# Kernel optimization log

Measured on AMD Instinct MI355X. Metric: run time of the kernel, lower is better.

## Reference

```python
import jax, jax.numpy as jnp
import numpy as np

B, S, D = 1, 4096, 1024
H = 16
DH = D // H  # 64
THETA = 10000.0


def setup_inputs() -> dict:
    key = jax.random.key(0)
    kq, kk, kv, kwq, kwk, kwv, kwo = jax.random.split(key, 7)
    scale = 0.02
    return {
        "q": jax.random.normal(kq, (B, S, D), dtype=jnp.float32),
        "k": jax.random.normal(kk, (B, S, D), dtype=jnp.float32),
        "v": jax.random.normal(kv, (B, S, D), dtype=jnp.float32),
        "Wq": jax.random.normal(kwq, (D, D), dtype=jnp.float32) * scale,
        "Wk": jax.random.normal(kwk, (D, D), dtype=jnp.float32) * scale,
        "Wv": jax.random.normal(kwv, (D, D), dtype=jnp.float32) * scale,
        "Wo": jax.random.normal(kwo, (D, D), dtype=jnp.float32) * scale,
        "bo": jnp.zeros((D,), dtype=jnp.float32),
    }


def _rope_tables(seq_len, d_head, dtype):
    # freqs_cis = polar(1, outer(t, 1/theta^(2i/d)))  -> cos/sin tables [seq, d_head//2]
    inv_freq = 1.0 / (THETA ** (jnp.arange(0, d_head, 2, dtype=jnp.float32) / d_head))
    ang = jnp.arange(seq_len, dtype=jnp.float32)[:, None] * inv_freq[None, :]
    return jnp.cos(ang).astype(dtype), jnp.sin(ang).astype(dtype)


def _apply_rope(x, cos, sin):
    # x: [B, S, H, DH]; pairs (even, odd) form complex numbers (xr + i*xi)
    xr = x[..., 0::2]
    xi = x[..., 1::2]
    c = cos[None, :, None, :]
    s = sin[None, :, None, :]
    out_r = xr * c - xi * s
    out_i = xr * s + xi * c
    # interleave back: [..., DH//2, 2] -> [..., DH]
    return jnp.stack([out_r, out_i], axis=-1).reshape(x.shape)


def reference(q, k, v, Wq, Wk, Wv, Wo, bo):
    b, sq, d = q.shape
    sk = k.shape[1]
    # torch nn.Linear: y = x @ W.T (no bias for q/k/v)
    xq = (q @ Wq.T).reshape(b, sq, H, DH)
    xk = (k @ Wk.T).reshape(b, sk, H, DH)
    xv = (v @ Wv.T).reshape(b, sk, H, DH)

    cos, sin = _rope_tables(max(sq, sk), DH, q.dtype)
    xq = _apply_rope(xq, cos[:sq], sin[:sq])
    xk = _apply_rope(xk, cos[:sk], sin[:sk])

    scale = 1.0 / np.sqrt(DH)
    # naive unfused attention (as in the source): full score matrix [B,H,Sq,Sk]
    scores = jnp.einsum("bqhd,bkhd->bhqk", xq, xk) * scale
    attn = jax.nn.softmax(scores, axis=-1)
    out = jnp.einsum("bhqk,bkhd->bqhd", attn, xv)
    out = out.reshape(b, sq, d)
    # output projection (with bias); dropout is identity in eval
    return out @ Wo.T + bo
```

## Files before the change

kernel.cpp:

```cpp
#include <hip/hip_runtime.h>
#include <hip/hip_bf16.h>
#include <math.h>

#define SQ 4096
#define DM 1024
#define NH 16

typedef unsigned int uint32;
typedef unsigned short u16;
typedef __attribute__((ext_vector_type(8))) __bf16 bf16x8;
typedef __attribute__((ext_vector_type(4))) __bf16 bf16x4;
typedef __attribute__((ext_vector_type(4))) float f32x4;
typedef __attribute__((ext_vector_type(4))) short s16x4;
typedef __attribute__((ext_vector_type(8))) unsigned short u16x8;
typedef __attribute__((ext_vector_type(4))) unsigned short u16x4;

__device__ __forceinline__ u16 f2bf(float f) {
  uint32 u = __builtin_bit_cast(uint32, f);
  u += 0x7FFFu + ((u >> 16) & 1u);
  return (u16)(u >> 16);
}

__device__ __forceinline__ void gld16(const void* g, void* l) {
  __builtin_amdgcn_global_load_lds((const __attribute__((address_space(1))) void*)g,
                                   (__attribute__((address_space(3))) void*)l, 16, 0, 0);
}

__device__ __forceinline__ f32x4 mfma32(bf16x8 a, bf16x8 b, f32x4 c) {
  return __builtin_amdgcn_mfma_f32_16x16x32_bf16(a, b, c, 0, 0, 0);
}

__device__ __forceinline__ f32x4 mfma16(s16x4 a, s16x4 b, f32x4 c) {
  return __builtin_amdgcn_mfma_f32_16x16x16bf16_1k(a, b, c, 0, 0, 0);
}

__global__ void cvt_kernel(const float* __restrict__ src, u16* __restrict__ dst, int n4, float scale) {
  int i = blockIdx.x * blockDim.x + threadIdx.x;
  if (i < n4) {
    float4 v = reinterpret_cast<const float4*>(src)[i];
    u16x4 o = { f2bf(v.x * scale), f2bf(v.y * scale), f2bf(v.z * scale), f2bf(v.w * scale) };
    reinterpret_cast<u16x4*>(dst)[i] = o;
  }
}

__global__ void rope_tab_kernel(float2* __restrict__ tab) {
  int t = blockIdx.x * blockDim.x + threadIdx.x;
  int s = t >> 5, p = t & 31;
  double inv = pow(10000.0, -(double)p / 32.0);
  float ang = (float)s * (float)inv;
  tab[t] = make_float2(cosf(ang), sinf(ang));
}

__device__ __forceinline__ void gemm_core(const u16* __restrict__ Ag, const u16* __restrict__ Bg,
                                          u16* As, u16* Bs, f32x4 (&acc)[4][4], int s0, int i0) {
  const int tid = threadIdx.x;
  const int lane = tid & 63;
  const int wv = tid >> 6;
  const int wr = wv >> 1, wc = wv & 1;
  const int r15 = lane & 15, g = lane >> 4;
  const int srow = tid >> 2;
  const int schk = (tid & 3) * 8;

  for (int k0 = 0; k0 < DM; k0 += 32) {
#pragma unroll
    for (int half = 0; half < 2; ++half) {
      gld16(Ag + (size_t)(s0 + half * 64 + srow) * DM + k0 + schk, As + (half * 256 + wv * 64) * 8);
      gld16(Bg + (size_t)(i0 + half * 64 + srow) * DM + k0 + schk, Bs + (half * 256 + wv * 64) * 8);
    }
    __syncthreads();
    bf16x8 af[4], bfr[4];
#pragma unroll
    for (int m = 0; m < 4; ++m)
      af[m] = *reinterpret_cast<const bf16x8*>(As + (wr * 64 + m * 16 + r15) * 32 + g * 8);
#pragma unroll
    for (int n = 0; n < 4; ++n)
      bfr[n] = *reinterpret_cast<const bf16x8*>(Bs + (wc * 64 + n * 16 + r15) * 32 + g * 8);
#pragma unroll
    for (int m = 0; m < 4; ++m)
#pragma unroll
      for (int n = 0; n < 4; ++n)
        acc[m][n] = mfma32(af[m], bfr[n], acc[m][n]);
    __syncthreads();
  }
}

__global__ __launch_bounds__(256) void proj_kernel(
    const u16* __restrict__ qb, const u16* __restrict__ kb, const u16* __restrict__ vb,
    const u16* __restrict__ Wq, const u16* __restrict__ Wk, const u16* __restrict__ Wv,
    u16* __restrict__ Xq, u16* __restrict__ Xk, u16* __restrict__ Vt,
    const float2* __restrict__ tab) {
  __shared__ u16 As[128 * 32], Bs[128 * 32];
  const int z = blockIdx.z;
  const u16* Ag = (z == 0) ? qb : (z == 1) ? kb : vb;
  const u16* Bg = (z == 0) ? Wq : (z == 1) ? Wk : Wv;
  const int s0 = blockIdx.x * 128, i0 = blockIdx.y * 128;
  f32x4 acc[4][4] = {};
  gemm_core(Ag, Bg, As, Bs, acc, s0, i0);

  const int tid = threadIdx.x, lane = tid & 63, wv = tid >> 6;
  const int wr = wv >> 1, wc = wv & 1, r15 = lane & 15, g = lane >> 4;
  if (z < 2) {
    u16* dst = (z == 0) ? Xq : Xk;
#pragma unroll
    for (int m = 0; m < 4; ++m) {
#pragma unroll
      for (int n = 0; n < 4; ++n) {
        int i = i0 + wc * 64 + n * 16 + r15;
        int p = (i & 63) >> 1;
#pragma unroll
        for (int r = 0; r < 4; ++r) {
          int s = s0 + wr * 64 + m * 16 + g * 4 + r;
          float v = acc[m][n][r];
          float o = __shfl_xor(v, 1);
          float2 cs = tab[s * 32 + p];
          float res = ((lane & 1) == 0) ? (v * cs.x - o * cs.y)
                                        : (o * cs.y + v * cs.x);
          dst[(size_t)s * DM + i] = f2bf(res);
        }
      }
    }
  } else {
#pragma unroll
    for (int m = 0; m < 4; ++m) {
#pragma unroll
      for (int n = 0; n < 4; ++n) {
        int i = i0 + wc * 64 + n * 16 + r15;
        int h = i >> 6, dh = i & 63;
        int sb = s0 + wr * 64 + m * 16 + g * 4;
        u16x4 pk = { f2bf(acc[m][n][0]), f2bf(acc[m][n][1]), f2bf(acc[m][n][2]), f2bf(acc[m][n][3]) };
        *reinterpret_cast<u16x4*>(Vt + (size_t)h * (64 * SQ) + (size_t)dh * SQ + sb) = pk;
      }
    }
  }
}

__global__ __launch_bounds__(256) void attn_kernel(const u16* __restrict__ Xq, const u16* __restrict__ Xk,
                                                   const u16* __restrict__ Vt, u16* __restrict__ Ob) {
  __shared__ u16 Ks[64 * 64], Vs[64 * 64];
  const int tid = threadIdx.x, lane = tid & 63, wv = tid >> 6;
  const int r15 = lane & 15, g = lane >> 4;
  const int h = blockIdx.y;
  const int q0 = blockIdx.x * 64 + wv * 16;

  bf16x8 qf[2];
#pragma unroll
  for (int kc = 0; kc < 2; ++kc)
    qf[kc] = *reinterpret_cast<const bf16x8*>(Xq + (size_t)(q0 + r15) * DM + h * 64 + kc * 32 + g * 8);

  f32x4 oacc[4] = {};
  float m_run = -3e38f, l_run = 0.f;

  u16x8 kst[2], vst[2];
  auto ldregs = [&](int t) {
#pragma unroll
    for (int j = 0; j < 2; ++j) {
      int c = tid + j * 256, row = c >> 3, ch = c & 7;
      kst[j] = *reinterpret_cast<const u16x8*>(Xk + (size_t)(t * 64 + row) * DM + h * 64 + ch * 8);
      vst[j] = *reinterpret_cast<const u16x8*>(Vt + (size_t)h * (64 * SQ) + (size_t)row * SQ + t * 64 + ch * 8);
    }
  };
  ldregs(0);

  for (int t = 0; t < 64; ++t) {
    __syncthreads();
#pragma unroll
    for (int j = 0; j < 2; ++j) {
      int c = tid + j * 256, row = c >> 3, ch = c & 7;
      int byt = (row * 128 + ch * 16) ^ ((row & 7) << 4);
      *reinterpret_cast<u16x8*>(reinterpret_cast<char*>(Ks) + byt) = kst[j];
      *reinterpret_cast<u16x8*>(reinterpret_cast<char*>(Vs) + byt) = vst[j];
    }
    __syncthreads();
    if (t < 63) ldregs(t + 1);

    f32x4 sa[4] = {};
#pragma unroll
    for (int kc = 0; kc < 2; ++kc) {
#pragma unroll
      for (int km = 0; km < 4; ++km) {
        int row = km * 16 + r15;
        int byt = (row * 128 + kc * 64 + g * 16) ^ ((row & 7) << 4);
        bf16x8 kf = *reinterpret_cast<const bf16x8*>(reinterpret_cast<const char*>(Ks) + byt);
        sa[km] = mfma32(kf, qf[kc], sa[km]);
      }
    }
    float mx = -3e38f;
#pragma unroll
    for (int km = 0; km < 4; ++km)
#pragma unroll
      for (int r = 0; r < 4; ++r) mx = fmaxf(mx, sa[km][r]);
    mx = fmaxf(mx, __shfl_xor(mx, 16));
    mx = fmaxf(mx, __shfl_xor(mx, 32));
    float mnew = fmaxf(m_run, mx);
    float p[16], psum = 0.f;
#pragma unroll
    for (int km = 0; km < 4; ++km)
#pragma unroll
      for (int r = 0; r < 4; ++r) {
        float e = __expf(sa[km][r] - mnew);
        p[km * 4 + r] = e;
        psum += e;
      }
    psum += __shfl_xor(psum, 16);
    psum += __shfl_xor(psum, 32);
    float fac = __expf(m_run - mnew);
    l_run = l_run * fac + psum;
    m_run = mnew;
#pragma unroll
    for (int r = 0; r < 4; ++r) {
      float fr = __shfl(fac, g * 4 + r);
#pragma unroll
      for (int n = 0; n < 4; ++n) oacc[n][r] *= fr;
    }
#pragma unroll
    for (int kk = 0; kk < 4; ++kk) {
      s16x4 pa = { (short)f2bf(p[kk * 4 + 0]), (short)f2bf(p[kk * 4 + 1]),
                   (short)f2bf(p[kk * 4 + 2]), (short)f2bf(p[kk * 4 + 3]) };
#pragma unroll
      for (int n = 0; n < 4; ++n) {
        int vrow = n * 16 + r15;
        int byt = (vrow * 128 + kk * 32 + g * 8) ^ ((vrow & 7) << 4);
        s16x4 vfr = *reinterpret_cast<const s16x4*>(reinterpret_cast<const char*>(Vs) + byt);
        oacc[n] = mfma16(pa, vfr, oacc[n]);
      }
    }
  }

  float linv = 1.f / l_run;
#pragma unroll
  for (int r = 0; r < 4; ++r) {
    float lr = __shfl(linv, g * 4 + r);
#pragma unroll
    for (int n = 0; n < 4; ++n) {
      int q = q0 + g * 4 + r;
      int dh = n * 16 + r15;
      Ob[(size_t)q * DM + h * 64 + dh] = f2bf(oacc[n][r] * lr);
    }
  }
}

__global__ __launch_bounds__(256) void out_kernel(const u16* __restrict__ Ob, const u16* __restrict__ Wo,
                                                  float* __restrict__ out, const float* __restrict__ bias) {
  __shared__ u16 As[128 * 32], Bs[128 * 32];
  const int s0 = blockIdx.x * 128, i0 = blockIdx.y * 128;
  f32x4 acc[4][4] = {};
  gemm_core(Ob, Wo, As, Bs, acc, s0, i0);
  const int tid = threadIdx.x, lane = tid & 63, wv = tid >> 6;
  const int wr = wv >> 1, wc = wv & 1, r15 = lane & 15, g = lane >> 4;
#pragma unroll
  for (int m = 0; m < 4; ++m) {
#pragma unroll
    for (int n = 0; n < 4; ++n) {
      int i = i0 + wc * 64 + n * 16 + r15;
      float bv = bias[i];
#pragma unroll
      for (int r = 0; r < 4; ++r) {
        int s = s0 + wr * 64 + m * 16 + g * 4 + r;
        out[(size_t)s * DM + i] = acc[m][n][r] + bv;
      }
    }
  }
}

extern "C" void kernel_launch(void* const* d_in, const int* in_sizes, int n_in,
                              void* d_out, int out_size, void* d_ws, size_t ws_size,
                              hipStream_t stream) {
  const float* q  = (const float*)d_in[0];
  const float* k  = (const float*)d_in[1];
  const float* v  = (const float*)d_in[2];
  const float* Wq = (const float*)d_in[3];
  const float* Wk = (const float*)d_in[4];
  const float* Wv = (const float*)d_in[5];
  const float* Wo = (const float*)d_in[6];
  const float* bo = (const float*)d_in[7];
  float* out = (float*)d_out;

  char* ws = (char*)d_ws;
  size_t off = 0;
  auto alloc = [&](size_t bytes) { char* p = ws + off; off += (bytes + 255) & ~(size_t)255; return p; };
  u16* qb  = (u16*)alloc((size_t)SQ * DM * 2);
  u16* kb  = (u16*)alloc((size_t)SQ * DM * 2);
  u16* vb  = (u16*)alloc((size_t)SQ * DM * 2);
  u16* Wqb = (u16*)alloc((size_t)DM * DM * 2);
  u16* Wkb = (u16*)alloc((size_t)DM * DM * 2);
  u16* Wvb = (u16*)alloc((size_t)DM * DM * 2);
  u16* Wob = (u16*)alloc((size_t)DM * DM * 2);
  u16* Xq  = (u16*)alloc((size_t)SQ * DM * 2);
  u16* Xk  = (u16*)alloc((size_t)SQ * DM * 2);
  u16* Vt  = (u16*)alloc((size_t)SQ * DM * 2);
  float2* tab = (float2*)alloc((size_t)SQ * 32 * sizeof(float2));
  u16* Ob = qb;

  const int nbig = SQ * DM / 4;
  const int nw = DM * DM / 4;
  cvt_kernel<<<nbig / 256, 256, 0, stream>>>(q, qb, nbig, 1.0f);
  cvt_kernel<<<nbig / 256, 256, 0, stream>>>(k, kb, nbig, 1.0f);
  cvt_kernel<<<nbig / 256, 256, 0, stream>>>(v, vb, nbig, 1.0f);
  cvt_kernel<<<nw / 256, 256, 0, stream>>>(Wq, Wqb, nw, 0.125f);
  cvt_kernel<<<nw / 256, 256, 0, stream>>>(Wk, Wkb, nw, 1.0f);
  cvt_kernel<<<nw / 256, 256, 0, stream>>>(Wv, Wvb, nw, 1.0f);
  cvt_kernel<<<nw / 256, 256, 0, stream>>>(Wo, Wob, nw, 1.0f);
  rope_tab_kernel<<<(SQ * 32) / 256, 256, 0, stream>>>(tab);

  proj_kernel<<<dim3(32, 8, 3), 256, 0, stream>>>(qb, kb, vb, Wqb, Wkb, Wvb, Xq, Xk, Vt, tab);
  attn_kernel<<<dim3(64, 16), 256, 0, stream>>>(Xq, Xk, Vt, Ob);
  out_kernel<<<dim3(32, 8), 256, 0, stream>>>(Ob, Wob, out, bo);
}
```

Before: 341.9 us.

## Fuse prep conversions, double-buffer attention LDS, lazy softmax rescale, exp2 and packed bf16

The eight conversion and rope-table launches become a single prep kernel. The query scale now folds in log2(e), so the attention softmax can use exp2f. The attention kernel double-buffers K/V in shared memory, which removes one barrier per tile and overlaps the LDS stores with compute. It also skips the running-max rescale unless the max grows by more than a threshold, and packs probabilities with a hardware bf16 pack instruction. The lazy rescale lets unnormalized values grow by up to 2^8 before rescaling, which carries some risk to numerical accuracy.

```diff
diff --git a/kernel.cpp b/kernel.cpp
--- a/kernel.cpp
+++ b/kernel.cpp
@@ -9,11 +9,11 @@
 typedef unsigned int uint32;
 typedef unsigned short u16;
 typedef __attribute__((ext_vector_type(8))) __bf16 bf16x8;
-typedef __attribute__((ext_vector_type(4))) __bf16 bf16x4;
 typedef __attribute__((ext_vector_type(4))) float f32x4;
 typedef __attribute__((ext_vector_type(4))) short s16x4;
 typedef __attribute__((ext_vector_type(8))) unsigned short u16x8;
 typedef __attribute__((ext_vector_type(4))) unsigned short u16x4;
+typedef __attribute__((ext_vector_type(2))) unsigned int u32x2;
 
 __device__ __forceinline__ u16 f2bf(float f) {
   uint32 u = __builtin_bit_cast(uint32, f);
@@ -21,6 +21,12 @@
   return (u16)(u >> 16);
 }
 
+__device__ __forceinline__ uint32 cvtpk(float a, float b) {
+  uint32 r;
+  asm("v_cvt_pk_bf16_f32 %0, %1, %2" : "=v"(r) : "v"(a), "v"(b));
+  return r;
+}
+
 __device__ __forceinline__ void gld16(const void* g, void* l) {
   __builtin_amdgcn_global_load_lds((const __attribute__((address_space(1))) void*)g,
                                    (__attribute__((address_space(3))) void*)l, 16, 0, 0);
@@ -34,21 +40,38 @@
   return __builtin_amdgcn_mfma_f32_16x16x16bf16_1k(a, b, c, 0, 0, 0);
 }
 
-__global__ void cvt_kernel(const float* __restrict__ src, u16* __restrict__ dst, int n4, float scale) {
-  int i = blockIdx.x * blockDim.x + threadIdx.x;
-  if (i < n4) {
-    float4 v = reinterpret_cast<const float4*>(src)[i];
-    u16x4 o = { f2bf(v.x * scale), f2bf(v.y * scale), f2bf(v.z * scale), f2bf(v.w * scale) };
-    reinterpret_cast<u16x4*>(dst)[i] = o;
-  }
-}
-
-__global__ void rope_tab_kernel(float2* __restrict__ tab) {
-  int t = blockIdx.x * blockDim.x + threadIdx.x;
-  int s = t >> 5, p = t & 31;
-  double inv = pow(10000.0, -(double)p / 32.0);
-  float ang = (float)s * (float)inv;
-  tab[t] = make_float2(cosf(ang), sinf(ang));
+#define QSCALE (0.125f * 1.44269504088896f)
+__global__ void prep_kernel(const float* __restrict__ q, const float* __restrict__ k, const float* __restrict__ v,
+                            const float* __restrict__ Wq, const float* __restrict__ Wk,
+                            const float* __restrict__ Wv, const float* __restrict__ Wo,
+                            u16* __restrict__ qb, u16* __restrict__ kb, u16* __restrict__ vb,
+                            u16* __restrict__ Wqb, u16* __restrict__ Wkb, u16* __restrict__ Wvb,
+                            u16* __restrict__ Wob, float2* __restrict__ tab) {
+  int b = blockIdx.x;
+  if (b < 12288) {
+    int r = b >> 12;
+    int i = (b & 4095) * 256 + threadIdx.x;
+    const float* s = (r == 0) ? q : (r == 1) ? k : v;
+    u16* d = (r == 0) ? qb : (r == 1) ? kb : vb;
+    float4 x = reinterpret_cast<const float4*>(s)[i];
+    u16x4 o = { f2bf(x.x), f2bf(x.y), f2bf(x.z), f2bf(x.w) };
+    reinterpret_cast<u16x4*>(d)[i] = o;
+  } else if (b < 16384) {
+    int w = (b - 12288) >> 10;
+    int i = ((b - 12288) & 1023) * 256 + threadIdx.x;
+    const float* s = (w == 0) ? Wq : (w == 1) ? Wk : (w == 2) ? Wv : Wo;
+    u16* d = (w == 0) ? Wqb : (w == 1) ? Wkb : (w == 2) ? Wvb : Wob;
+    float sc = (w == 0) ? QSCALE : 1.0f;
+    float4 x = reinterpret_cast<const float4*>(s)[i];
+    u16x4 o = { f2bf(x.x * sc), f2bf(x.y * sc), f2bf(x.z * sc), f2bf(x.w * sc) };
+    reinterpret_cast<u16x4*>(d)[i] = o;
+  } else {
+    int t = (b - 16384) * 256 + threadIdx.x;
+    int s = t >> 5, p = t & 31;
+    double inv = pow(10000.0, -(double)p / 32.0);
+    float ang = (float)s * (float)inv;
+    tab[t] = make_float2(cosf(ang), sinf(ang));
+  }
 }
 
 __device__ __forceinline__ void gemm_core(const u16* __restrict__ Ag, const u16* __restrict__ Bg,
@@ -136,7 +159,7 @@
 
 __global__ __launch_bounds__(256) void attn_kernel(const u16* __restrict__ Xq, const u16* __restrict__ Xk,
                                                    const u16* __restrict__ Vt, u16* __restrict__ Ob) {
-  __shared__ u16 Ks[64 * 64], Vs[64 * 64];
+  __shared__ u16 Ks[2][64 * 64], Vs[2][64 * 64];
   const int tid = threadIdx.x, lane = tid & 63, wv = tid >> 6;
   const int r15 = lane & 15, g = lane >> 4;
   const int h = blockIdx.y;
@@ -150,77 +173,103 @@
   f32x4 oacc[4] = {};
   float m_run = -3e38f, l_run = 0.f;
 
+  const int row0 = tid >> 3, ch0 = tid & 7;
+  const int row1 = (tid + 256) >> 3, ch1 = tid & 7;
+  const u16* Kg0 = Xk + (size_t)row0 * DM + h * 64 + ch0 * 8;
+  const u16* Kg1 = Xk + (size_t)row1 * DM + h * 64 + ch1 * 8;
+  const u16* Vg0 = Vt + (size_t)h * (64 * SQ) + (size_t)row0 * SQ + ch0 * 8;
+  const u16* Vg1 = Vt + (size_t)h * (64 * SQ) + (size_t)row1 * SQ + ch1 * 8;
+  const int wb0 = (row0 * 128 + ch0 * 16) ^ ((row0 & 7) << 4);
+  const int wb1 = (row1 * 128 + ch1 * 16) ^ ((row1 & 7) << 4);
+  const int xr = (r15 & 7) << 4;
+
   u16x8 kst[2], vst[2];
   auto ldregs = [&](int t) {
-#pragma unroll
-    for (int j = 0; j < 2; ++j) {
-      int c = tid + j * 256, row = c >> 3, ch = c & 7;
-      kst[j] = *reinterpret_cast<const u16x8*>(Xk + (size_t)(t * 64 + row) * DM + h * 64 + ch * 8);
-      vst[j] = *reinterpret_cast<const u16x8*>(Vt + (size_t)h * (64 * SQ) + (size_t)row * SQ + t * 64 + ch * 8);
-    }
+    kst[0] = *reinterpret_cast<const u16x8*>(Kg0 + (size_t)t * 64 * DM);
+    kst[1] = *reinterpret_cast<const u16x8*>(Kg1 + (size_t)t * 64 * DM);
+    vst[0] = *reinterpret_cast<const u16x8*>(Vg0 + t * 64);
+    vst[1] = *reinterpret_cast<const u16x8*>(Vg1 + t * 64);
   };
+
   ldregs(0);
+  {
+    char* Kw = (char*)Ks[0]; char* Vw = (char*)Vs[0];
+    *reinterpret_cast<u16x8*>(Kw + wb0) = kst[0];
+    *reinterpret_cast<u16x8*>(Kw + wb1) = kst[1];
+    *reinterpret_cast<u16x8*>(Vw + wb0) = vst[0];
+    *reinterpret_cast<u16x8*>(Vw + wb1) = vst[1];
+  }
 
   for (int t = 0; t < 64; ++t) {
     __syncthreads();
-#pragma unroll
-    for (int j = 0; j < 2; ++j) {
-      int c = tid + j * 256, row = c >> 3, ch = c & 7;
-      int byt = (row * 128 + ch * 16) ^ ((row & 7) << 4);
-      *reinterpret_cast<u16x8*>(reinterpret_cast<char*>(Ks) + byt) = kst[j];
-      *reinterpret_cast<u16x8*>(reinterpret_cast<char*>(Vs) + byt) = vst[j];
-    }
-    __syncthreads();
     if (t < 63) ldregs(t + 1);
+    const char* Kb = (const char*)Ks[t & 1];
+    const char* Vb = (const char*)Vs[t & 1];
 
     f32x4 sa[4] = {};
 #pragma unroll
-    for (int kc = 0; kc < 2; ++kc) {
+    for (int kc = 0; kc < 2; ++kc)
 #pragma unroll
       for (int km = 0; km < 4; ++km) {
-        int row = km * 16 + r15;
-        int byt = (row * 128 + kc * 64 + g * 16) ^ ((row & 7) << 4);
-        bf16x8 kf = *reinterpret_cast<const bf16x8*>(reinterpret_cast<const char*>(Ks) + byt);
+        int byt = ((km * 16 + r15) * 128 + kc * 64 + g * 16) ^ xr;
+        bf16x8 kf = *reinterpret_cast<const bf16x8*>(Kb + byt);
         sa[km] = mfma32(kf, qf[kc], sa[km]);
       }
-    }
-    float mx = -3e38f;
+
+    float mx = sa[0][0];
 #pragma unroll
     for (int km = 0; km < 4; ++km)
 #pragma unroll
       for (int r = 0; r < 4; ++r) mx = fmaxf(mx, sa[km][r]);
     mx = fmaxf(mx, __shfl_xor(mx, 16));
     mx = fmaxf(mx, __shfl_xor(mx, 32));
-    float mnew = fmaxf(m_run, mx);
+
+    if (!__all(mx <= m_run + 8.f)) {
+      float mnew = fmaxf(m_run, mx);
+      float fac = exp2f(m_run - mnew);
+      m_run = mnew;
+      l_run *= fac;
+#pragma unroll
+      for (int r = 0; r < 4; ++r) {
+        float fr = __shfl(fac, g * 4 + r);
+#pragma unroll
+        for (int n = 0; n < 4; ++n) oacc[n][r] *= fr;
+      }
+    }
+
     float p[16], psum = 0.f;
 #pragma unroll
     for (int km = 0; km < 4; ++km)
 #pragma unroll
       for (int r = 0; r < 4; ++r) {
-        float e = __expf(sa[km][r] - mnew);
+        float e = exp2f(sa[km][r] - m_run);
         p[km * 4 + r] = e;
         psum += e;
       }
     psum += __shfl_xor(psum, 16);
     psum += __shfl_xor(psum, 32);
-    float fac = __expf(m_run - mnew);
-    l_run = l_run * fac + psum;
-    m_run = mnew;
-#pragma unroll
-    for (int r = 0; r < 4; ++r) {
-      float fr = __shfl(fac, g * 4 + r);
-#pragma unroll
-      for (int n = 0; n < 4; ++n) oacc[n][r] *= fr;
-    }
+    l_run += psum;
+
+    uint32 pw[8];
+#pragma unroll
+    for (int i = 0; i < 8; ++i) pw[i] = cvtpk(p[2 * i], p[2 * i + 1]);
+
+    if (t < 63) {
+      char* Kw = (char*)Ks[(t + 1) & 1]; char* Vw = (char*)Vs[(t + 1) & 1];
+      *reinterpret_cast<u16x8*>(Kw + wb0) = kst[0];
+      *reinterpret_cast<u16x8*>(Kw + wb1) = kst[1];
+      *reinterpret_cast<u16x8*>(Vw + wb0) = vst[0];
+      *reinterpret_cast<u16x8*>(Vw + wb1) = vst[1];
+    }
+
 #pragma unroll
     for (int kk = 0; kk < 4; ++kk) {
-      s16x4 pa = { (short)f2bf(p[kk * 4 + 0]), (short)f2bf(p[kk * 4 + 1]),
-                   (short)f2bf(p[kk * 4 + 2]), (short)f2bf(p[kk * 4 + 3]) };
+      u32x2 w; w.x = pw[2 * kk]; w.y = pw[2 * kk + 1];
+      s16x4 pa = __builtin_bit_cast(s16x4, w);
 #pragma unroll
       for (int n = 0; n < 4; ++n) {
-        int vrow = n * 16 + r15;
-        int byt = (vrow * 128 + kk * 32 + g * 8) ^ ((vrow & 7) << 4);
-        s16x4 vfr = *reinterpret_cast<const s16x4*>(reinterpret_cast<const char*>(Vs) + byt);
+        int byt = ((n * 16 + r15) * 128 + kk * 32 + g * 8) ^ xr;
+        s16x4 vfr = *reinterpret_cast<const s16x4*>(Vb + byt);
         oacc[n] = mfma16(pa, vfr, oacc[n]);
       }
     }
@@ -232,9 +281,9 @@
     float lr = __shfl(linv, g * 4 + r);
 #pragma unroll
     for (int n = 0; n < 4; ++n) {
-      int q = q0 + g * 4 + r;
+      int qq = q0 + g * 4 + r;
       int dh = n * 16 + r15;
-      Ob[(size_t)q * DM + h * 64 + dh] = f2bf(oacc[n][r] * lr);
+      Ob[(size_t)qq * DM + h * 64 + dh] = f2bf(oacc[n][r] * lr);
     }
   }
 }
@@ -291,17 +340,8 @@
   float2* tab = (float2*)alloc((size_t)SQ * 32 * sizeof(float2));
   u16* Ob = qb;
 
-  const int nbig = SQ * DM / 4;
-  const int nw = DM * DM / 4;
-  cvt_kernel<<<nbig / 256, 256, 0, stream>>>(q, qb, nbig, 1.0f);
-  cvt_kernel<<<nbig / 256, 256, 0, stream>>>(k, kb, nbig, 1.0f);
-  cvt_kernel<<<nbig / 256, 256, 0, stream>>>(v, vb, nbig, 1.0f);
-  cvt_kernel<<<nw / 256, 256, 0, stream>>>(Wq, Wqb, nw, 0.125f);
-  cvt_kernel<<<nw / 256, 256, 0, stream>>>(Wk, Wkb, nw, 1.0f);
-  cvt_kernel<<<nw / 256, 256, 0, stream>>>(Wv, Wvb, nw, 1.0f);
-  cvt_kernel<<<nw / 256, 256, 0, stream>>>(Wo, Wob, nw, 1.0f);
-  rope_tab_kernel<<<(SQ * 32) / 256, 256, 0, stream>>>(tab);
-
+  prep_kernel<<<16896, 256, 0, stream>>>(q, k, v, Wq, Wk, Wv, Wo,
+                                         qb, kb, vb, Wqb, Wkb, Wvb, Wob, tab);
   proj_kernel<<<dim3(32, 8, 3), 256, 0, stream>>>(qb, kb, vb, Wqb, Wkb, Wvb, Xq, Xk, Vt, tab);
   attn_kernel<<<dim3(64, 16), 256, 0, stream>>>(Xq, Xk, Vt, Ob);
   out_kernel<<<dim3(32, 8), 256, 0, stream>>>(Ob, Wob, out, bo);
```

Result: slower. 357.0 us (+4.4%).
